# Performance work log

Measured on AMD Instinct MI355X. Metric: run time of the kernel, lower is better.

## Reference

```python
import jax, jax.numpy as jnp
import numpy as np

H, W = 64, 64          # self.shape = (W, H) = (64, 64)
REG_MAX = 16
TOPK = 4

def _dwconv(y, w, b):
    # y: (N, L, C) -> depthwise 3x3 conv on (N, C, H, W) -> (N, L, C)
    N, L, C = y.shape
    img = jnp.transpose(y, (0, 2, 1)).reshape(N, C, H, W)
    out = jax.lax.conv_general_dilated(
        img, w, (1, 1), ((1, 1), (1, 1)),
        dimension_numbers=('NCHW', 'OIHW', 'NCHW'), feature_group_count=C)
    out = out + b[None, :, None, None]
    return jnp.transpose(out.reshape(N, C, H * W), (0, 2, 1))

def _mlp(x, fc1_w, fc1_b, dw1_w, dw1_b, fc2_w, fc2_b, dw2_w, dw2_b, fc3_w, fc3_b):
    h = x @ fc1_w.T + fc1_b
    h = jax.nn.gelu(_dwconv(h, dw1_w, dw1_b), approximate=False)  # torch nn.GELU is exact erf
    h = h @ fc2_w.T + fc2_b
    h = jax.nn.gelu(_dwconv(h, dw2_w, dw2_b), approximate=False)
    return h @ fc3_w.T + fc3_b

def setup_inputs() -> dict:
    key = jax.random.key(0)
    ks = iter(jax.random.split(key, 16))
    d = {}
    d['x'] = jax.random.normal(next(ks), (1, 32, H * W, 256), dtype=jnp.float32)
    for p in ('c_', 'r_'):
        out3 = 1 if p == 'c_' else 4 * (REG_MAX + 1)
        d[p + 'fc1_w'] = 0.02 * jax.random.normal(next(ks), (256, 256), dtype=jnp.float32)
        d[p + 'fc1_b'] = jnp.zeros((256,), jnp.float32)
        d[p + 'dw1_w'] = 0.3 * jax.random.normal(next(ks), (256, 1, 3, 3), dtype=jnp.float32)
        d[p + 'dw1_b'] = jnp.zeros((256,), jnp.float32)
        d[p + 'fc2_w'] = 0.02 * jax.random.normal(next(ks), (256, 256), dtype=jnp.float32)
        d[p + 'fc2_b'] = jnp.zeros((256,), jnp.float32)
        d[p + 'dw2_w'] = 0.3 * jax.random.normal(next(ks), (256, 1, 3, 3), dtype=jnp.float32)
        d[p + 'dw2_b'] = jnp.zeros((256,), jnp.float32)
        d[p + 'fc3_w'] = 0.02 * jax.random.normal(next(ks), (out3, 256), dtype=jnp.float32)
        d[p + 'fc3_b'] = jnp.zeros((out3,), jnp.float32)
    d['rc1_w'] = 0.1 * jax.random.normal(next(ks), (64, 4 * (TOPK + 1)), dtype=jnp.float32)
    d['rc1_b'] = jnp.zeros((64,), jnp.float32)
    d['rc2_w'] = 0.1 * jax.random.normal(next(ks), (1, 64), dtype=jnp.float32)
    d['rc2_b'] = jnp.zeros((1,), jnp.float32)
    return d

def reference(x,
              c_fc1_w, c_fc1_b, c_dw1_w, c_dw1_b, c_fc2_w, c_fc2_b, c_dw2_w, c_dw2_b, c_fc3_w, c_fc3_b,
              r_fc1_w, r_fc1_b, r_dw1_w, r_dw1_b, r_fc2_w, r_fc2_b, r_dw2_w, r_dw2_b, r_fc3_w, r_fc3_b,
              rc1_w, rc1_b, rc2_w, rc2_b):
    xs = x[0]                                   # (N, L, C)
    N = xs.shape[0]
    reg_pred = _mlp(xs, r_fc1_w, r_fc1_b, r_dw1_w, r_dw1_b, r_fc2_w, r_fc2_b,
                    r_dw2_w, r_dw2_b, r_fc3_w, r_fc3_b)  # (N, L, 4*(reg_max+1))
    prob = jax.nn.softmax(
        jnp.transpose(reg_pred, (0, 2, 1)).reshape(N, 4, REG_MAX + 1, H, W), axis=2)
    pt = jnp.transpose(prob, (0, 1, 3, 4, 2))   # (N,4,H,W,reg_max+1)
    topk, _ = jax.lax.top_k(pt, TOPK)           # (N,4,H,W,topk), sorted desc like torch
    stat = jnp.concatenate([topk, topk.mean(axis=-1, keepdims=True)], axis=-1)
    stat = jnp.transpose(stat, (0, 1, 4, 2, 3)).reshape(N, 4 * (TOPK + 1), H, W)
    q = jax.nn.relu(jnp.einsum('nchw,oc->nohw', stat, rc1_w) + rc1_b[None, :, None, None])
    q = jax.nn.sigmoid(jnp.einsum('nchw,oc->nohw', q, rc2_w) + rc2_b[None, :, None, None])
    cls = _mlp(xs, c_fc1_w, c_fc1_b, c_dw1_w, c_dw1_b, c_fc2_w, c_fc2_b,
               c_dw2_w, c_dw2_b, c_fc3_w, c_fc3_b)      # (N, L, 1)
    cls = jax.nn.sigmoid(jnp.transpose(cls, (0, 2, 1)).reshape(N, 1, H, W)) * q
    proj = jnp.arange(REG_MAX + 1, dtype=reg_pred.dtype)  # linspace(0, reg_max, reg_max+1)
    dist = jax.nn.softmax(reg_pred.reshape(-1, REG_MAX + 1), axis=1) @ proj
    boxes = dist.reshape(N, H, W, 4) / REG_MAX
    return cls, boxes, reg_pred.reshape(N, H, W, 4 * (REG_MAX + 1))
```

## Files before the change

kernel.cpp:

```cpp
#include <hip/hip_runtime.h>
#include <hip/hip_bf16.h>

typedef __bf16 bf16x8 __attribute__((ext_vector_type(8)));
typedef float f32x4 __attribute__((ext_vector_type(4)));
typedef float f32x2 __attribute__((ext_vector_type(2)));

__device__ __forceinline__ float bf2f(unsigned short b) {
  unsigned int u = ((unsigned int)b) << 16;
  return __builtin_bit_cast(float, u);
}
__device__ __forceinline__ unsigned short f2bf(float f) {
  unsigned int u = __builtin_bit_cast(unsigned int, f);
  unsigned int r = u + 0x7fffu + ((u >> 16) & 1u);
  return (unsigned short)(r >> 16);
}
__device__ __forceinline__ f32x2 unpack2(unsigned int u) {
  f32x2 r;
  r.x = __builtin_bit_cast(float, u << 16);
  r.y = __builtin_bit_cast(float, u & 0xffff0000u);
  return r;
}

__device__ __forceinline__ void gload16(const void* g, void* l) {
  typedef __attribute__((address_space(1))) const void* gp_t;
  typedef __attribute__((address_space(3))) void* lp_t;
  __builtin_amdgcn_global_load_lds((gp_t)g, (lp_t)l, 16, 0, 0);
}

__device__ __forceinline__ f32x2 gelu2(f32x2 x) {
  f32x2 m = x * x;
  f32x2 t = m * (-0.10295273f) + (-2.3021967f);
  f32x2 u = x * t;
  f32x2 e;
  e.x = __builtin_amdgcn_exp2f(u.x);
  e.y = __builtin_amdgcn_exp2f(u.y);
  f32x2 d = e + 1.0f;
  f32x2 r;
  r.x = __builtin_amdgcn_rcpf(d.x);
  r.y = __builtin_amdgcn_rcpf(d.y);
  return x * r;
}
__device__ __forceinline__ unsigned int cvt_pk_bf16(float lo, float hi) {
  unsigned int r;
  asm("v_cvt_pk_bf16_f32 %0, %1, %2" : "=v"(r) : "v"(lo), "v"(hi));
  return r;
}

__global__ __launch_bounds__(256) void cvt_x(const float* __restrict__ in,
                                             unsigned short* __restrict__ out) {
  long i = ((long)blockIdx.x * 256 + threadIdx.x) * 8;
  float4 a = *(const float4*)(in + i);
  float4 b = *(const float4*)(in + i + 4);
  __align__(16) unsigned short o[8];
  o[0] = f2bf(a.x); o[1] = f2bf(a.y); o[2] = f2bf(a.z); o[3] = f2bf(a.w);
  o[4] = f2bf(b.x); o[5] = f2bf(b.y); o[6] = f2bf(b.z); o[7] = f2bf(b.w);
  *(uint4*)(out + i) = *(uint4*)o;
}

__global__ __launch_bounds__(256) void prep_all(
    const float* __restrict__ c1w, const float* __restrict__ r1w,
    const float* __restrict__ c2w, const float* __restrict__ r2w,
    const float* __restrict__ c3w, const float* __restrict__ r3w, const float* __restrict__ r3b,
    const float* __restrict__ c1b, const float* __restrict__ r1b,
    const float* __restrict__ c2b, const float* __restrict__ r2b,
    const float* __restrict__ d1wc, const float* __restrict__ d1bc,
    const float* __restrict__ d1wr, const float* __restrict__ d1br,
    const float* __restrict__ d2wc, const float* __restrict__ d2bc,
    const float* __restrict__ d2wr, const float* __restrict__ d2br,
    unsigned short* __restrict__ w1cat, unsigned short* __restrict__ w2cat,
    unsigned short* __restrict__ c3wb, unsigned short* __restrict__ wr3pad,
    float* __restrict__ br3pad, float* __restrict__ b1cat, float* __restrict__ b2cat,
    float* __restrict__ wd1, float* __restrict__ bd1,
    float* __restrict__ wd2, float* __restrict__ bd2) {
  int i = blockIdx.x * 256 + threadIdx.x;
  {
    int which = i >> 16, j = i & 65535;
    float v = (which == 0) ? c1w[j] : (which == 1) ? r1w[j] : (which == 2) ? c2w[j] : r2w[j];
    unsigned short* dst = (which < 2) ? (w1cat + which * 65536) : (w2cat + (which - 2) * 65536);
    dst[j] = f2bf(v);
  }
  if (i < 32768) {
    int r = i >> 8, c = i & 255;
    wr3pad[i] = (r < 68) ? f2bf(r3w[r * 256 + c]) : (unsigned short)0;
    if (i < 128) br3pad[i] = (i < 68) ? r3b[i] : 0.f;
  }
  if (i < 256) c3wb[i] = f2bf(c3w[i]);
  if (i < 4608) {
    int tap = i >> 9, ch = i & 511, cc = ch & 255;
    wd1[i] = (ch < 256) ? d1wc[cc * 9 + tap] : d1wr[cc * 9 + tap];
    wd2[i] = (ch < 256) ? d2wc[cc * 9 + tap] : d2wr[cc * 9 + tap];
  }
  if (i < 512) {
    bd1[i] = (i < 256) ? d1bc[i] : d1br[i & 255];
    bd2[i] = (i < 256) ? d2bc[i] : d2br[i & 255];
    b1cat[i] = (i < 256) ? c1b[i] : r1b[i & 255];
    b2cat[i] = (i < 256) ? c2b[i] : r2b[i & 255];
  }
}

__global__ __launch_bounds__(256, 3) void gemm_glds(
    const unsigned short* __restrict__ A, int lda, int zAoff,
    const unsigned short* __restrict__ W, int zWoff,
    const float* __restrict__ bias, int zBoff,
    unsigned short* __restrict__ Out, int ldo, int zOoff, int lnN,
    float* __restrict__ OutF) {
  __shared__ unsigned short lds[2][8192];
  const int z = blockIdx.z;
  const unsigned short* Az = A + (long)z * zAoff;
  const unsigned short* Wz = W + (long)z * zWoff;
  const float* biasz = bias + z * zBoff;
  unsigned short* Outz = Out + (long)z * zOoff;

  const int nwg = gridDim.x;
  const int bid = blockIdx.x;
  const int wg = (bid & 7) * (nwg >> 3) + (bid >> 3);
  const int mtile = wg >> lnN;
  const int ntile = wg & ((1 << lnN) - 1);
  const long row0 = (long)mtile * 128;
  const int col0 = ntile * 128;

  const int tid = threadIdx.x;
  const int lane = tid & 63;
  const int wid = tid >> 6;
  const int wr = (wid >> 1) * 64;
  const int wc = (wid & 1) * 64;
  const int rr = lane & 15;
  const int gk = lane >> 4;
  const int swz = (rr >> 1) & 3;

  const int srow_l = (wid << 4) + (lane >> 2);
  const int sgl = lane & 3;

  f32x4 acc[4][4] = {};

  auto stage = [&](int buf, int k0) {
    #pragma unroll
    for (int j = 0; j < 4; j++) {
      const int slotbase = j * 256 + (wid << 6);
      unsigned short* ldst = &lds[buf][slotbase * 8];
      const int row = (j & 1) * 64 + srow_l;
      const int g = sgl ^ ((row >> 1) & 3);
      const unsigned short* src;
      if (j < 2) src = Az + (row0 + row) * (long)lda + k0 + g * 8;
      else       src = Wz + (long)(col0 + row) * 256 + k0 + g * 8;
      gload16(src, ldst);
    }
  };

  stage(0, 0);
  #pragma unroll
  for (int ks = 0; ks < 8; ks++) {
    if (ks < 7) {
      stage((ks + 1) & 1, (ks + 1) * 32);
      asm volatile("s_waitcnt vmcnt(4)" ::: "memory");
    } else {
      asm volatile("s_waitcnt vmcnt(0)" ::: "memory");
    }
    __builtin_amdgcn_s_barrier();
    asm volatile("" ::: "memory");
    const unsigned short* buf = lds[ks & 1];
    bf16x8 af[4], bf[4];
    #pragma unroll
    for (int mi = 0; mi < 4; mi++)
      af[mi] = __builtin_bit_cast(bf16x8,
          *(const uint4*)&buf[(wr + mi * 16 + rr) * 32 + ((gk ^ swz) * 8)]);
    #pragma unroll
    for (int ni = 0; ni < 4; ni++)
      bf[ni] = __builtin_bit_cast(bf16x8,
          *(const uint4*)&buf[4096 + (wc + ni * 16 + rr) * 32 + ((gk ^ swz) * 8)]);
    #pragma unroll
    for (int mi = 0; mi < 4; mi++)
      #pragma unroll
      for (int ni = 0; ni < 4; ni++)
        acc[mi][ni] = __builtin_amdgcn_mfma_f32_16x16x32_bf16(af[mi], bf[ni], acc[mi][ni], 0, 0, 0);
    asm volatile("" ::: "memory");
    __builtin_amdgcn_s_barrier();
  }

  #pragma unroll
  for (int mi = 0; mi < 4; mi++) {
    const int rbase = wr + mi * 16 + (lane >> 4) * 4;
    #pragma unroll
    for (int ni = 0; ni < 4; ni++) {
      const int c_ = wc + ni * 16 + (lane & 15);
      const float bv = biasz[col0 + c_];
      #pragma unroll
      for (int r = 0; r < 4; r++) {
        const float val = acc[mi][ni][r] + bv;
        Outz[(row0 + rbase + r) * (long)ldo + col0 + c_] = f2bf(val);
        if (OutF != nullptr && c_ < 68)
          OutF[(row0 + rbase + r) * 68L + c_] = val;
      }
    }
  }
}

template <bool CLS>
__global__ __launch_bounds__(256) void dwconv_gelu4(
    const unsigned short* __restrict__ In,
    const float* __restrict__ Wt, const float* __restrict__ Bt,
    unsigned short* __restrict__ Out,
    const unsigned short* __restrict__ Wc3, const float* __restrict__ bc3,
    float* __restrict__ cls_logit) {
  const int t = blockIdx.x * 256 + threadIdx.x;
  const int g = t & 63;
  const int p = t >> 6;
  const int n = p >> 10;
  const int h = (p >> 4) & 63;
  const int w0 = (p & 15) << 2;
  const int cbase = g << 3;
  f32x2 acc[4][4];
  {
    float4 b0 = *(const float4*)(Bt + cbase);
    float4 b1 = *(const float4*)(Bt + cbase + 4);
    f32x2 bb[4];
    bb[0].x = b0.x; bb[0].y = b0.y; bb[1].x = b0.z; bb[1].y = b0.w;
    bb[2].x = b1.x; bb[2].y = b1.y; bb[3].x = b1.z; bb[3].y = b1.w;
    #pragma unroll
    for (int k = 0; k < 4; k++)
      #pragma unroll
      for (int i = 0; i < 4; i++) acc[k][i] = bb[i];
  }
  #pragma unroll
  for (int dy = -1; dy <= 1; dy++) {
    const int hh = h + dy;
    if (hh < 0 || hh > 63) continue;
    const float* wbase = Wt + ((dy + 1) * 3) * 512 + cbase;
    f32x2 wt[3][4];
    #pragma unroll
    for (int j = 0; j < 3; j++) {
      float4 a0 = *(const float4*)(wbase + j * 512);
      float4 a1 = *(const float4*)(wbase + j * 512 + 4);
      wt[j][0].x = a0.x; wt[j][0].y = a0.y; wt[j][1].x = a0.z; wt[j][1].y = a0.w;
      wt[j][2].x = a1.x; wt[j][2].y = a1.y; wt[j][3].x = a1.z; wt[j][3].y = a1.w;
    }
    const long rowtok = (long)(((n << 6) + hh) << 6);
    f32x2 f[6][4];
    #pragma unroll
    for (int d = 0; d < 6; d++) {
      const int col = w0 - 1 + d;
      uint4 v = {0u, 0u, 0u, 0u};
      if (col >= 0 && col < 64)
        v = *(const uint4*)(In + (rowtok + col) * 512 + cbase);
      f[d][0] = unpack2(v.x); f[d][1] = unpack2(v.y);
      f[d][2] = unpack2(v.z); f[d][3] = unpack2(v.w);
    }
    #pragma unroll
    for (int k = 0; k < 4; k++)
      #pragma unroll
      for (int j = 0; j < 3; j++)
        #pragma unroll
        for (int i = 0; i < 4; i++)
          acc[k][i] += f[k + j][i] * wt[j][i];
  }
  f32x2 w3[4];
  if (CLS) {
    const int cc = cbase & 255;
    uint4 wv = *(const uint4*)(Wc3 + cc);
    w3[0] = unpack2(wv.x); w3[1] = unpack2(wv.y);
    w3[2] = unpack2(wv.z); w3[3] = unpack2(wv.w);
  }
  const long mbase = ((long)((n << 6) + h) << 6) + w0;
  float s[4];
  #pragma unroll
  for (int k = 0; k < 4; k++) {
    __align__(16) unsigned int ov[4];
    f32x2 ge[4];
    #pragma unroll
    for (int i = 0; i < 4; i++) {
      ge[i] = gelu2(acc[k][i]);
      ov[i] = cvt_pk_bf16(ge[i].x, ge[i].y);
    }
    if (!CLS || cbase >= 256)
      *(uint4*)(Out + (mbase + k) * 512 + cbase) = *(uint4*)ov;
    if (CLS) {
      f32x2 sp = ge[0] * w3[0] + ge[1] * w3[1] + ge[2] * w3[2] + ge[3] * w3[3];
      s[k] = sp.x + sp.y;
    }
  }
  if (CLS) {
    #pragma unroll
    for (int k = 0; k < 4; k++) {
      #pragma unroll
      for (int m = 16; m >= 1; m >>= 1) s[k] += __shfl_xor(s[k], m);
    }
    if (g == 0) {
      float b = bc3[0];
      float4 o;
      o.x = s[0] + b; o.y = s[1] + b; o.z = s[2] + b; o.w = s[3] + b;
      *(float4*)(cls_logit + mbase) = o;
    }
  }
}

__global__ __launch_bounds__(256) void post_kernel(
    const unsigned short* __restrict__ RP,
    const float* __restrict__ cls_logit,
    const float* __restrict__ rc1_w, const float* __restrict__ rc1_b,
    const float* __restrict__ rc2_w, const float* __restrict__ rc2_b,
    float* __restrict__ out_cls, float* __restrict__ out_boxes) {
  int m = blockIdx.x * 256 + threadIdx.x;
  const unsigned short* rp = RP + (long)m * 128;
  __align__(16) unsigned short raw[72];
  #pragma unroll
  for (int q = 0; q < 9; q++)
    *(uint4*)(raw + q * 8) = *(const uint4*)(rp + q * 8);
  float stat[20];
  float4 boxes;
  #pragma unroll
  for (int s = 0; s < 4; s++) {
    float v[17];
    float mx = -1e30f;
    #pragma unroll
    for (int i = 0; i < 17; i++) {
      v[i] = bf2f(raw[s * 17 + i]);
      mx = fmaxf(mx, v[i]);
    }
    float sum = 0.f;
    #pragma unroll
    for (int i = 0; i < 17; i++) { v[i] = __expf(v[i] - mx); sum += v[i]; }
    float inv = 1.f / sum;
    float dist = 0.f;
    #pragma unroll
    for (int i = 0; i < 17; i++) { v[i] *= inv; dist += v[i] * (float)i; }
    ((float*)&boxes)[s] = dist * 0.0625f;
    float tk[4];
    #pragma unroll
    for (int t = 0; t < 4; t++) {
      float bm = v[0]; int bi = 0;
      #pragma unroll
      for (int i = 1; i < 17; i++) {
        if (v[i] > bm) { bm = v[i]; bi = i; }
      }
      tk[t] = bm;
      #pragma unroll
      for (int i = 0; i < 17; i++)
        if (i == bi) v[i] = -1.f;
    }
    stat[s * 5 + 0] = tk[0]; stat[s * 5 + 1] = tk[1];
    stat[s * 5 + 2] = tk[2]; stat[s * 5 + 3] = tk[3];
    stat[s * 5 + 4] = 0.25f * (tk[0] + tk[1] + tk[2] + tk[3]);
  }
  *(float4*)(out_boxes + (long)m * 4) = boxes;
  float z = 0.f;
  #pragma unroll
  for (int o = 0; o < 64; o++) {
    float q = rc1_b[o];
    #pragma unroll
    for (int c = 0; c < 20; c++) q += rc1_w[o * 20 + c] * stat[c];
    q = fmaxf(q, 0.f);
    z += q * rc2_w[o];
  }
  z += rc2_b[0];
  float q2 = 1.f / (1.f + __expf(-z));
  float cl = 1.f / (1.f + __expf(-cls_logit[m]));
  out_cls[m] = cl * q2;
}

extern "C" void kernel_launch(void* const* d_in, const int* in_sizes, int n_in,
                              void* d_out, int out_size, void* d_ws, size_t ws_size,
                              hipStream_t stream) {
  const float* x       = (const float*)d_in[0];
  const float* c_fc1_w = (const float*)d_in[1];
  const float* c_fc1_b = (const float*)d_in[2];
  const float* c_dw1_w = (const float*)d_in[3];
  const float* c_dw1_b = (const float*)d_in[4];
  const float* c_fc2_w = (const float*)d_in[5];
  const float* c_fc2_b = (const float*)d_in[6];
  const float* c_dw2_w = (const float*)d_in[7];
  const float* c_dw2_b = (const float*)d_in[8];
  const float* c_fc3_w = (const float*)d_in[9];
  const float* c_fc3_b = (const float*)d_in[10];
  const float* r_fc1_w = (const float*)d_in[11];
  const float* r_fc1_b = (const float*)d_in[12];
  const float* r_dw1_w = (const float*)d_in[13];
  const float* r_dw1_b = (const float*)d_in[14];
  const float* r_fc2_w = (const float*)d_in[15];
  const float* r_fc2_b = (const float*)d_in[16];
  const float* r_dw2_w = (const float*)d_in[17];
  const float* r_dw2_b = (const float*)d_in[18];
  const float* r_fc3_w = (const float*)d_in[19];
  const float* r_fc3_b = (const float*)d_in[20];
  const float* rc1_w   = (const float*)d_in[21];
  const float* rc1_b   = (const float*)d_in[22];
  const float* rc2_w   = (const float*)d_in[23];
  const float* rc2_b   = (const float*)d_in[24];

  char* ws = (char*)d_ws;
  unsigned short* Hbuf = (unsigned short*)ws;
  unsigned short* Gbuf = (unsigned short*)(ws + 134217728L);
  unsigned short* xb   = Gbuf;
  unsigned short* RP   = (unsigned short*)(ws + 268435456L);
  float* cls_logit     = (float*)(ws + 301989888L);
  char* wb             = ws + 302514176L;
  unsigned short* w1cat  = (unsigned short*)wb;
  unsigned short* w2cat  = w1cat + 131072;
  unsigned short* c3wb   = w2cat + 131072;
  unsigned short* wr3pad = c3wb + 256;
  float* br3pad = (float*)(wr3pad + 32768);
  float* b1cat  = br3pad + 128;
  float* b2cat  = b1cat + 512;
  float* wd1    = b2cat + 512;
  float* bd1    = wd1 + 4608;
  float* wd2    = bd1 + 512;
  float* bd2    = wd2 + 4608;

  float* out_cls   = (float*)d_out;
  float* out_boxes = out_cls + 131072;
  float* out_reg   = out_boxes + 524288;

  prep_all<<<1024, 256, 0, stream>>>(
      c_fc1_w, r_fc1_w, c_fc2_w, r_fc2_w, c_fc3_w, r_fc3_w, r_fc3_b,
      c_fc1_b, r_fc1_b, c_fc2_b, r_fc2_b,
      c_dw1_w, c_dw1_b, r_dw1_w, r_dw1_b,
      c_dw2_w, c_dw2_b, r_dw2_w, r_dw2_b,
      w1cat, w2cat, c3wb, wr3pad, br3pad, b1cat, b2cat,
      wd1, bd1, wd2, bd2);
  cvt_x<<<16384, 256, 0, stream>>>(x, xb);

  gemm_glds<<<dim3(4096, 1, 1), 256, 0, stream>>>(
      xb, 256, 0, w1cat, 0, b1cat, 0, Hbuf, 512, 0, 2, nullptr);
  dwconv_gelu4<false><<<8192, 256, 0, stream>>>(Hbuf, wd1, bd1, Gbuf,
                                                nullptr, nullptr, nullptr);
  gemm_glds<<<dim3(2048, 1, 2), 256, 0, stream>>>(
      Gbuf, 512, 256, w2cat, 65536, b2cat, 256, Hbuf, 512, 256, 1, nullptr);
  dwconv_gelu4<true><<<8192, 256, 0, stream>>>(Hbuf, wd2, bd2, Gbuf,
                                               c3wb, c_fc3_b, cls_logit);
  gemm_glds<<<dim3(1024, 1, 1), 256, 0, stream>>>(
      Gbuf + 256, 512, 0, wr3pad, 0, br3pad, 0, RP, 128, 0, 0, out_reg);
  post_kernel<<<512, 256, 0, stream>>>(RP, cls_logit, rc1_w, rc1_b, rc2_w, rc2_b,
                                       out_cls, out_boxes);
}
```

Before: 349.2 us.

## Fuse fp32-to-bf16 input conversion into the first GEMM's A-tile load

Removes the standalone cvt_x kernel and adds a new GEMM kernel that reads fp32 x directly, converts it to bf16 in registers and stores the full 128x256 A tile swizzled into LDS, while only the W tiles are double-buffered. This avoids writing and re-reading a 64 MB bf16 copy of x plus one kernel launch. In exchange the kernel uses more LDS (a 64 KB A tile), runs at a lower occupancy bound of 2, and each A tile row is re-read from fp32 across the four N tiles instead of from the half-size bf16 copy.

```diff
diff --git a/kernel.cpp b/kernel.cpp
--- a/kernel.cpp
+++ b/kernel.cpp
@@ -44,17 +44,6 @@
   unsigned int r;
   asm("v_cvt_pk_bf16_f32 %0, %1, %2" : "=v"(r) : "v"(lo), "v"(hi));
   return r;
-}
-
-__global__ __launch_bounds__(256) void cvt_x(const float* __restrict__ in,
-                                             unsigned short* __restrict__ out) {
-  long i = ((long)blockIdx.x * 256 + threadIdx.x) * 8;
-  float4 a = *(const float4*)(in + i);
-  float4 b = *(const float4*)(in + i + 4);
-  __align__(16) unsigned short o[8];
-  o[0] = f2bf(a.x); o[1] = f2bf(a.y); o[2] = f2bf(a.z); o[3] = f2bf(a.w);
-  o[4] = f2bf(b.x); o[5] = f2bf(b.y); o[6] = f2bf(b.z); o[7] = f2bf(b.w);
-  *(uint4*)(out + i) = *(uint4*)o;
 }
 
 __global__ __launch_bounds__(256) void prep_all(
@@ -95,6 +84,113 @@
     bd2[i] = (i < 256) ? d2bc[i] : d2br[i & 255];
     b1cat[i] = (i < 256) ? c1b[i] : r1b[i & 255];
     b2cat[i] = (i < 256) ? c2b[i] : r2b[i & 255];
+  }
+}
+
+__global__ __launch_bounds__(256, 2) void gemm_f32a(
+    const float* __restrict__ X,
+    const unsigned short* __restrict__ W,
+    const float* __restrict__ bias,
+    unsigned short* __restrict__ Out, int ldo, int lnN) {
+  __shared__ unsigned short ldsA[32768];
+  __shared__ unsigned short ldsB[2][4096];
+  const int nwg = gridDim.x;
+  const int bid = blockIdx.x;
+  const int wg = (bid & 7) * (nwg >> 3) + (bid >> 3);
+  const int mtile = wg >> lnN;
+  const int ntile = wg & ((1 << lnN) - 1);
+  const long row0 = (long)mtile * 128;
+  const int col0 = ntile * 128;
+
+  const int tid = threadIdx.x;
+  const int lane = tid & 63;
+  const int wid = tid >> 6;
+  const int wr = (wid >> 1) * 64;
+  const int wc = (wid & 1) * 64;
+  const int rr = lane & 15;
+  const int gk = lane >> 4;
+  const int swz = (rr >> 1) & 3;
+
+  const int srow_l = (wid << 4) + (lane >> 2);
+  const int sgl = lane & 3;
+
+  {
+    const int arow = tid >> 1;
+    const int cpart = tid & 1;
+    const float* src = X + (row0 + arow) * 256L + cpart * 128;
+    const int rswz = (arow >> 1) & 3;
+    #pragma unroll 4
+    for (int j = 0; j < 16; j++) {
+      const int glog = cpart * 16 + j;
+      const float4 v0 = *(const float4*)(src + j * 8);
+      const float4 v1 = *(const float4*)(src + j * 8 + 4);
+      uint4 pk;
+      pk.x = cvt_pk_bf16(v0.x, v0.y);
+      pk.y = cvt_pk_bf16(v0.z, v0.w);
+      pk.z = cvt_pk_bf16(v1.x, v1.y);
+      pk.w = cvt_pk_bf16(v1.z, v1.w);
+      const int phys = (glog & ~3) | ((glog & 3) ^ rswz);
+      *(uint4*)&ldsA[(arow * 32 + phys) * 8] = pk;
+    }
+  }
+
+  auto stageB = [&](int buf, int k0) {
+    #pragma unroll
+    for (int j = 0; j < 2; j++) {
+      const int slotbase = j * 256 + (wid << 6);
+      const int row = j * 64 + srow_l;
+      const int g = sgl ^ ((row >> 1) & 3);
+      gload16(W + (long)(col0 + row) * 256 + k0 + g * 8,
+              &ldsB[buf][slotbase * 8]);
+    }
+  };
+
+  f32x4 acc[4][4] = {};
+  stageB(0, 0);
+  asm volatile("s_waitcnt vmcnt(0) lgkmcnt(0)" ::: "memory");
+  __builtin_amdgcn_s_barrier();
+
+  #pragma unroll
+  for (int ks = 0; ks < 8; ks++) {
+    if (ks < 7) {
+      stageB((ks + 1) & 1, (ks + 1) * 32);
+      asm volatile("s_waitcnt vmcnt(2)" ::: "memory");
+    } else {
+      asm volatile("s_waitcnt vmcnt(0)" ::: "memory");
+    }
+    __builtin_amdgcn_s_barrier();
+    asm volatile("" ::: "memory");
+    const unsigned short* bufB = ldsB[ks & 1];
+    bf16x8 af[4], bf[4];
+    #pragma unroll
+    for (int mi = 0; mi < 4; mi++)
+      af[mi] = __builtin_bit_cast(bf16x8,
+          *(const uint4*)&ldsA[((wr + mi * 16 + rr) * 32 + ks * 4 + (gk ^ swz)) * 8]);
+    #pragma unroll
+    for (int ni = 0; ni < 4; ni++)
+      bf[ni] = __builtin_bit_cast(bf16x8,
+          *(const uint4*)&bufB[((wc + ni * 16 + rr) * 4 + (gk ^ swz)) * 8]);
+    #pragma unroll
+    for (int mi = 0; mi < 4; mi++)
+      #pragma unroll
+      for (int ni = 0; ni < 4; ni++)
+        acc[mi][ni] = __builtin_amdgcn_mfma_f32_16x16x32_bf16(af[mi], bf[ni], acc[mi][ni], 0, 0, 0);
+    asm volatile("" ::: "memory");
+    __builtin_amdgcn_s_barrier();
+  }
+
+  #pragma unroll
+  for (int mi = 0; mi < 4; mi++) {
+    const int rbase = wr + mi * 16 + (lane >> 4) * 4;
+    #pragma unroll
+    for (int ni = 0; ni < 4; ni++) {
+      const int c_ = wc + ni * 16 + (lane & 15);
+      const float bv = bias[col0 + c_];
+      #pragma unroll
+      for (int r = 0; r < 4; r++) {
+        Out[(row0 + rbase + r) * (long)ldo + col0 + c_] = f2bf(acc[mi][ni][r] + bv);
+      }
+    }
   }
 }
 
@@ -389,7 +485,6 @@
   char* ws = (char*)d_ws;
   unsigned short* Hbuf = (unsigned short*)ws;
   unsigned short* Gbuf = (unsigned short*)(ws + 134217728L);
-  unsigned short* xb   = Gbuf;
   unsigned short* RP   = (unsigned short*)(ws + 268435456L);
   float* cls_logit     = (float*)(ws + 301989888L);
   char* wb             = ws + 302514176L;
@@ -416,10 +511,9 @@
       c_dw2_w, c_dw2_b, r_dw2_w, r_dw2_b,
       w1cat, w2cat, c3wb, wr3pad, br3pad, b1cat, b2cat,
       wd1, bd1, wd2, bd2);
-  cvt_x<<<16384, 256, 0, stream>>>(x, xb);
-
-  gemm_glds<<<dim3(4096, 1, 1), 256, 0, stream>>>(
-      xb, 256, 0, w1cat, 0, b1cat, 0, Hbuf, 512, 0, 2, nullptr);
+
+  gemm_f32a<<<dim3(4096, 1, 1), 256, 0, stream>>>(
+      x, w1cat, b1cat, Hbuf, 512, 2);
   dwconv_gelu4<false><<<8192, 256, 0, stream>>>(Hbuf, wd1, bd1, Gbuf,
                                                 nullptr, nullptr, nullptr);
   gemm_glds<<<dim3(2048, 1, 2), 256, 0, stream>>>(
```

Result: slower. 393.0 us (+12.6%).
